# Performance work log

Hardware: AMD Instinct MI355X
Metric: run time of the kernel (lower is better)

The kernel has to match this reference:

```python
import jax, jax.numpy as jnp
from jax import lax
import numpy as np

NUM_HEADS = 16
NUM_HEADS_KV = 4
HEAD_DIM = 128
D_CONV = 4
ROT_DIM = 128
ROT_BASE = 10000.0
CAUSAL = True


def setup_inputs() -> dict:
    key = jax.random.key(0)
    ks = jax.random.split(key, 7)
    B, S, E = 2, 2048, 2048
    QKV = HEAD_DIM * (NUM_HEADS + 2 * NUM_HEADS_KV)  # 3072
    return {
        "x": jax.random.normal(ks[0], (B, S, E), jnp.float32),
        "W_in": jax.random.normal(ks[1], (QKV, E), jnp.float32) * 0.02,
        "b_in": jax.random.normal(ks[2], (QKV,), jnp.float32) * 0.02,
        "conv_w": jax.random.normal(ks[3], (QKV, D_CONV), jnp.float32) * 0.1,
        "conv_b": jax.random.normal(ks[4], (QKV,), jnp.float32) * 0.02,
        "W_out": jax.random.normal(ks[5], (E, NUM_HEADS * HEAD_DIM), jnp.float32) * 0.02,
        "b_out": jax.random.normal(ks[6], (E,), jnp.float32) * 0.02,
    }


def _rotary(x, cos, sin):
    # x: [B,S,H,D], non-interleaved rotary over first ROT_DIM dims (here full D)
    x1, x2 = x[..., : ROT_DIM // 2], x[..., ROT_DIM // 2 : ROT_DIM]
    c = cos[None, :, None, :]
    s = sin[None, :, None, :]
    rot = jnp.concatenate([x1 * c - x2 * s, x2 * c + x1 * s], axis=-1)
    return jnp.concatenate([rot, x[..., ROT_DIM:]], axis=-1)


def reference(x, W_in, b_in, conv_w, conv_b, W_out, b_out):
    B, S, E = x.shape
    QKV = conv_w.shape[0]
    # fused in-projection
    qkv = jnp.einsum("bse,fe->bsf", x, W_in) + b_in  # [B,S,QKV]
    # depthwise causal conv1d (left pad d_conv-1, equivalent to torch pad+trim)
    qkv_t = jnp.transpose(qkv, (0, 2, 1))  # [B,C,S]
    qkv_t = jnp.pad(qkv_t, ((0, 0), (0, 0), (D_CONV - 1, 0)))
    conv = lax.conv_general_dilated(
        qkv_t, conv_w[:, None, :], window_strides=(1,), padding="VALID",
        feature_group_count=QKV, dimension_numbers=("NCH", "OIH", "NCH"))
    qkv = jnp.transpose(conv + conv_b[None, :, None], (0, 2, 1))  # [B,S,QKV]
    # split q / kv
    q_dim = NUM_HEADS * HEAD_DIM
    q = qkv[..., :q_dim].reshape(B, S, NUM_HEADS, HEAD_DIM)
    kv = qkv[..., q_dim:].reshape(B, S, 2, NUM_HEADS_KV, HEAD_DIM)
    k, v = kv[:, :, 0], kv[:, :, 1]
    # rotary embedding on q and k
    t = jnp.arange(S, dtype=jnp.float32)
    inv_freq = 1.0 / (ROT_BASE ** (jnp.arange(0, ROT_DIM, 2, dtype=jnp.float32) / ROT_DIM))
    freqs = t[:, None] * inv_freq[None, :]  # [S, ROT_DIM/2]
    cos, sin = jnp.cos(freqs), jnp.sin(freqs)
    q = _rotary(q, cos, sin)
    k = _rotary(k, cos, sin)
    # GQA: repeat kv heads
    rep = NUM_HEADS // NUM_HEADS_KV
    k = jnp.repeat(k, rep, axis=2)  # [B,S,H,D]
    v = jnp.repeat(v, rep, axis=2)
    scale = 1.0 / jnp.sqrt(jnp.float32(HEAD_DIM))
    scores = jnp.einsum("bshd,bthd->bhst", q, k) * scale  # [B,H,S,S]
    if CAUSAL:
        mask = jnp.tril(jnp.ones((S, S), dtype=bool))
        scores = jnp.where(mask[None, None], scores, jnp.finfo(scores.dtype).min)
    attn = jax.nn.softmax(scores, axis=-1)
    ctx = jnp.einsum("bhst,bthd->bshd", attn, v).reshape(B, S, q_dim)
    return jnp.einsum("bsf,ef->bse", ctx, W_out) + b_out
```

## Files before the change

### kernel.cpp

```cpp
#include <hip/hip_runtime.h>
#include <hip/hip_bf16.h>

#define B_   2
#define S_   2048
#define E_   2048
#define QKV_ 3072
#define NH   16
#define NKV  4
#define HD   128
#define SL   16

typedef __attribute__((ext_vector_type(8))) short bf16x8;
typedef __attribute__((ext_vector_type(4))) float f32x4;
typedef unsigned short u16;
typedef unsigned int   u32;

__device__ __forceinline__ float bf2f(u16 u) {
  union { u32 i; float f; } v; v.i = ((u32)u) << 16; return v.f;
}
__device__ __forceinline__ u16 f2bf(float f) {
  union { float f; u32 u; } v; v.f = f;
  return (u16)((v.u + 0x7FFFu + ((v.u >> 16) & 1u)) >> 16);
}
__device__ __forceinline__ u32 pkbf(float a, float b) {
  __hip_bfloat162 h = __float22bfloat162_rn(float2{a, b});
  u32 r; __builtin_memcpy(&r, &h, 4); return r;
}
__device__ __forceinline__ float ex2(float x) { return __builtin_amdgcn_exp2f(x); }
__device__ __forceinline__ u32 shf(u32 v, int l) { return (u32)__shfl((int)v, l); }
__device__ __forceinline__ void load_lds16(const u16* g, u16* l) {
  __builtin_amdgcn_global_load_lds((const __attribute__((address_space(1))) void*)g,
                                   (__attribute__((address_space(3))) void*)l, 16, 0, 0);
}

__global__ __launch_bounds__(256) void f2b3(const float* __restrict__ x,
                                            const float* __restrict__ wi,
                                            const float* __restrict__ wo,
                                            u16* __restrict__ xb,
                                            u16* __restrict__ wib,
                                            u16* __restrict__ wob) {
  const int i = blockIdx.x * 256 + threadIdx.x;
  const float* src; u16* dst; int j;
  if (i < 2097152)            { src = x;  dst = xb;  j = i; }
  else if (i < 2097152 + 1572864) { src = wi; dst = wib; j = i - 2097152; }
  else                        { src = wo; dst = wob; j = i - 3670016; }
  const float4 v = ((const float4*)src)[j];
  ushort4 o;
  o.x = f2bf(v.x); o.y = f2bf(v.y); o.z = f2bf(v.z); o.w = f2bf(v.w);
  ((ushort4*)dst)[j] = o;
}

template <int OUT_BF16>
__global__ __launch_bounds__(512, 2) void gemm256(const u16* __restrict__ A,
                                                  const u16* __restrict__ Bm,
                                                  const float* __restrict__ bias,
                                                  void* __restrict__ C,
                                                  int M, int N, int K) {
  __shared__ u16 sm[2][2][256 * 64];
  const int tid = threadIdx.x;
  const int lane = tid & 63;
  const int wave = tid >> 6;
  const int wm = wave >> 2, wn = wave & 3;
  const int L15 = lane & 15, Lq = lane >> 4;
  const int m0 = blockIdx.y * 256, n0 = blockIdx.x * 256;
  const int NT = K >> 6;

  const int srow = tid >> 3;
  const int sdst = (tid & 7) * 8;
  const int ssrc = ((tid & 7) ^ (srow & 7)) * 8;

  f32x4 acc[8][4] = {};
  bf16x8 af[4][2], bf0[2][2], bf1[2][2];

#define STAGE_A(BUF, TC, H, J)                                                    \
  { const int row_ = (H) * 128 + (J) * 64 + srow;                                 \
    load_lds16(A + (size_t)(m0 + row_) * K + (TC) * 64 + ssrc,                    \
               &sm[BUF][0][row_ * 64 + sdst]); }
#define STAGE_B(BUF, TC, H, J)                                                    \
  { const int row_ = (H) * 128 + (J) * 64 + srow;                                 \
    load_lds16(Bm + (size_t)(n0 + row_) * K + (TC) * 64 + ssrc,                   \
               &sm[BUF][1][row_ * 64 + sdst]); }
#define RD_A(BUF, MS, MF, KK)                                                     \
  (*(const bf16x8*)&sm[BUF][0][(wm * 128 + (MS) * 64 + (MF) * 16 + L15) * 64 +    \
        ((((KK) * 4 + Lq) ^ ((wm * 128 + (MS) * 64 + (MF) * 16 + L15) & 7)) * 8)])
#define RD_B(BUF, NS, NF, KK)                                                     \
  (*(const bf16x8*)&sm[BUF][1][(wn * 64 + (NS) * 32 + (NF) * 16 + L15) * 64 +     \
        ((((KK) * 4 + Lq) ^ ((wn * 64 + (NS) * 32 + (NF) * 16 + L15) & 7)) * 8)])

#define MFMA_QUAD(MS, NS, BF)                                                     \
  __builtin_amdgcn_s_setprio(1);                                                  \
  _Pragma("unroll")                                                               \
  for (int kk = 0; kk < 2; ++kk)                                                  \
    _Pragma("unroll")                                                             \
    for (int mf = 0; mf < 4; ++mf)                                                \
      _Pragma("unroll")                                                           \
      for (int nf = 0; nf < 2; ++nf)                                              \
        acc[MS * 4 + mf][NS * 2 + nf] = __builtin_amdgcn_mfma_f32_16x16x32_bf16(  \
            af[mf][kk], BF[nf][kk], acc[MS * 4 + mf][NS * 2 + nf], 0, 0, 0);      \
  __builtin_amdgcn_s_setprio(0);

#define TILE_BODY(BUF, TT)                                                        \
  {                                                                               \
    _Pragma("unroll")                                                             \
    for (int mf = 0; mf < 4; ++mf)                                                \
      _Pragma("unroll")                                                           \
      for (int kk = 0; kk < 2; ++kk) af[mf][kk] = RD_A(BUF, 0, mf, kk);           \
    _Pragma("unroll")                                                             \
    for (int nf = 0; nf < 2; ++nf)                                                \
      _Pragma("unroll")                                                           \
      for (int kk = 0; kk < 2; ++kk) bf0[nf][kk] = RD_B(BUF, 0, nf, kk);          \
    if ((TT) + 1 < NT) { STAGE_A(BUF ^ 1, (TT) + 1, 1, 0)                         \
                         STAGE_A(BUF ^ 1, (TT) + 1, 1, 1) }                       \
    __builtin_amdgcn_s_barrier();                                                 \
    MFMA_QUAD(0, 0, bf0)                                                          \
    __builtin_amdgcn_s_barrier();                                                 \
    _Pragma("unroll")                                                             \
    for (int nf = 0; nf < 2; ++nf)                                                \
      _Pragma("unroll")                                                           \
      for (int kk = 0; kk < 2; ++kk) bf1[nf][kk] = RD_B(BUF, 1, nf, kk);          \
    if ((TT) + 1 < NT) { STAGE_B(BUF ^ 1, (TT) + 1, 1, 0)                         \
                         STAGE_B(BUF ^ 1, (TT) + 1, 1, 1) }                       \
    __builtin_amdgcn_s_barrier();                                                 \
    MFMA_QUAD(0, 1, bf1)                                                          \
    __builtin_amdgcn_s_barrier();                                                 \
    _Pragma("unroll")                                                             \
    for (int mf = 0; mf < 4; ++mf)                                                \
      _Pragma("unroll")                                                           \
      for (int kk = 0; kk < 2; ++kk) af[mf][kk] = RD_A(BUF, 1, mf, kk);           \
    if ((TT) + 2 < NT) { STAGE_B(BUF, (TT) + 2, 0, 0)                             \
                         STAGE_B(BUF, (TT) + 2, 0, 1) }                           \
    __builtin_amdgcn_s_barrier();                                                 \
    MFMA_QUAD(1, 0, bf0)                                                          \
    __builtin_amdgcn_s_barrier();                                                 \
    if ((TT) + 2 < NT) {                                                          \
      STAGE_A(BUF, (TT) + 2, 0, 0)                                                \
      STAGE_A(BUF, (TT) + 2, 0, 1)                                                \
      asm volatile("s_waitcnt vmcnt(4)" ::: "memory");                            \
    } else {                                                                      \
      asm volatile("s_waitcnt vmcnt(0)" ::: "memory");                            \
    }                                                                             \
    __builtin_amdgcn_s_barrier();                                                 \
    MFMA_QUAD(1, 1, bf1)                                                          \
    __builtin_amdgcn_s_barrier();                                                 \
  }

  STAGE_A(0, 0, 0, 0) STAGE_A(0, 0, 0, 1)
  STAGE_B(0, 0, 0, 0) STAGE_B(0, 0, 0, 1)
  STAGE_A(0, 0, 1, 0) STAGE_A(0, 0, 1, 1)
  STAGE_B(0, 0, 1, 0) STAGE_B(0, 0, 1, 1)
  STAGE_B(1, 1, 0, 0) STAGE_B(1, 1, 0, 1)
  STAGE_A(1, 1, 0, 0) STAGE_A(1, 1, 0, 1)
  asm volatile("s_waitcnt vmcnt(4)" ::: "memory");
  __builtin_amdgcn_s_barrier();

  for (int T = 0; T < NT; T += 2) {
    TILE_BODY(0, T)
    TILE_BODY(1, T + 1)
  }
#undef TILE_BODY
#undef MFMA_QUAD
#undef RD_B
#undef RD_A
#undef STAGE_B
#undef STAGE_A

#pragma unroll
  for (int ms = 0; ms < 2; ++ms)
#pragma unroll
    for (int mf = 0; mf < 4; ++mf) {
      const int grow0 = m0 + wm * 128 + ms * 64 + mf * 16 + Lq * 4;
#pragma unroll
      for (int ns = 0; ns < 2; ++ns)
#pragma unroll
        for (int nf = 0; nf < 2; ++nf) {
          const int gcol = n0 + wn * 64 + ns * 32 + nf * 16 + L15;
          const float bv = bias[gcol];
          const f32x4 v = acc[ms * 4 + mf][ns * 2 + nf];
#pragma unroll
          for (int r = 0; r < 4; ++r) {
            const float o = v[r] + bv;
            if (OUT_BF16) ((u16*)C)[(size_t)(grow0 + r) * N + gcol] = f2bf(o);
            else          ((float*)C)[(size_t)(grow0 + r) * N + gcol] = o;
          }
        }
    }
}

__global__ __launch_bounds__(512, 2) void gemm_n128(const u16* __restrict__ A,
                                                    const u16* __restrict__ Bm,
                                                    const float* __restrict__ bias,
                                                    float* __restrict__ C,
                                                    int M, int N, int K) {
  __shared__ u16 sm[2][24576];
  const int tid = threadIdx.x, lane = tid & 63, wave = tid >> 6;
  const int wm = wave >> 1, wn = wave & 1;
  const int L15 = lane & 15, Lq = lane >> 4;
  const int m0 = blockIdx.y * 256, n0 = blockIdx.x * 128;
  const int NT = K >> 6;

  const int srow = tid >> 3;
  const int sdst = (tid & 7) * 8;
  const int ssrc = ((tid & 7) ^ (srow & 7)) * 8;

  f32x4 acc[4][4] = {};

#define STAGE6(BUF, TC)                                                           \
  {                                                                               \
    _Pragma("unroll")                                                             \
    for (int c = 0; c < 4; ++c) {                                                 \
      const int row_ = c * 64 + srow;                                             \
      load_lds16(A + (size_t)(m0 + row_) * K + (TC) * 64 + ssrc,                  \
                 &sm[BUF][row_ * 64 + sdst]);                                     \
    }                                                                             \
    _Pragma("unroll")                                                             \
    for (int c = 0; c < 2; ++c) {                                                 \
      const int row_ = c * 64 + srow;                                             \
      load_lds16(Bm + (size_t)(n0 + row_) * K + (TC) * 64 + ssrc,                 \
                 &sm[BUF][16384 + row_ * 64 + sdst]);                             \
    }                                                                             \
  }

#define COMPUTE(BUF)                                                              \
  {                                                                               \
    bf16x8 af[4][2], bfr[4][2];                                                   \
    _Pragma("unroll")                                                             \
    for (int mf = 0; mf < 4; ++mf)                                                \
      _Pragma("unroll")                                                           \
      for (int kk = 0; kk < 2; ++kk) {                                            \
        const int row_ = wm * 64 + mf * 16 + L15;                                 \
        const int u_ = (kk * 4 + Lq) ^ (row_ & 7);                                \
        af[mf][kk] = *(const bf16x8*)&sm[BUF][row_ * 64 + u_ * 8];                \
      }                                                                           \
    _Pragma("unroll")                                                             \
    for (int nf = 0; nf < 4; ++nf)                                                \
      _Pragma("unroll")                                                           \
      for (int kk = 0; kk < 2; ++kk) {                                            \
        const int row_ = wn * 64 + nf * 16 + L15;                                 \
        const int u_ = (kk * 4 + Lq) ^ (row_ & 7);                                \
        bfr[nf][kk] = *(const bf16x8*)&sm[BUF][16384 + row_ * 64 + u_ * 8];       \
      }                                                                           \
    __builtin_amdgcn_s_setprio(1);                                                \
    _Pragma("unroll")                                                             \
    for (int kk = 0; kk < 2; ++kk)                                                \
      _Pragma("unroll")                                                           \
      for (int mf = 0; mf < 4; ++mf)                                              \
        _Pragma("unroll")                                                         \
        for (int nf = 0; nf < 4; ++nf)                                            \
          acc[mf][nf] = __builtin_amdgcn_mfma_f32_16x16x32_bf16(                  \
              af[mf][kk], bfr[nf][kk], acc[mf][nf], 0, 0, 0);                     \
    __builtin_amdgcn_s_setprio(0);                                                \
    __builtin_amdgcn_s_barrier();                                                 \
  }

  STAGE6(0, 0)
  for (int T = 0; T < NT; T += 2) {
    if (T + 1 < NT) {
      STAGE6(1, T + 1)
      asm volatile("s_waitcnt vmcnt(6)" ::: "memory");
    } else {
      asm volatile("s_waitcnt vmcnt(0)" ::: "memory");
    }
    __builtin_amdgcn_s_barrier();
    COMPUTE(0)
    if (T + 2 < NT) {
      STAGE6(0, T + 2)
      asm volatile("s_waitcnt vmcnt(6)" ::: "memory");
    } else {
      asm volatile("s_waitcnt vmcnt(0)" ::: "memory");
    }
    __builtin_amdgcn_s_barrier();
    COMPUTE(1)
  }
#undef COMPUTE
#undef STAGE6

#pragma unroll
  for (int mf = 0; mf < 4; ++mf) {
    const int grow0 = m0 + wm * 64 + mf * 16 + Lq * 4;
#pragma unroll
    for (int nf = 0; nf < 4; ++nf) {
      const int gcol = n0 + wn * 64 + nf * 16 + L15;
      const float bv = bias[gcol];
#pragma unroll
      for (int r = 0; r < 4; ++r)
        C[(size_t)(grow0 + r) * N + gcol] = acc[mf][nf][r] + bv;
    }
  }
}

__global__ __launch_bounds__(256) void conv_rope(const u16* __restrict__ qkv,
                                                 const float* __restrict__ cw,
                                                 const float* __restrict__ cb,
                                                 u16* __restrict__ qo,
                                                 u16* __restrict__ ko,
                                                 u16* __restrict__ vtmp) {
  const int blk = blockIdx.x;
  const int b = blk >> 7;
  const int s0 = (blk & 127) * SL;
  const u16* qb = qkv + (size_t)b * S_ * QKV_;

  for (int u = threadIdx.x; u < 896; u += 256) {
    if (u < 640) {
      const int hs = u >> 5, ip = u & 31, i = ip * 2;
      int f1; u16* outbase; float scale;
      if (hs < 16) {
        f1 = hs * HD + i;
        outbase = qo + (size_t)(b * NH + hs) * S_ * HD;
        scale = 0.08838834764831845f * 1.4426950408889634f;
      } else {
        f1 = NH * HD + (hs - 16) * HD + i;
        outbase = ko + (size_t)(b * NKV + (hs - 16)) * S_ * HD;
        scale = 1.0f;
      }
      const float invf0 = powf(10000.0f, -(float)i * (1.0f / 64.0f));
      const float invf1 = powf(10000.0f, -(float)(i + 1) * (1.0f / 64.0f));
      const int f2 = f1 + 64;
      const float4 wA0 = *(const float4*)&cw[f1 * 4];
      const float4 wA1 = *(const float4*)&cw[(f1 + 1) * 4];
      const float4 wB0 = *(const float4*)&cw[f2 * 4];
      const float4 wB1 = *(const float4*)&cw[(f2 + 1) * 4];
      const float cA0 = cb[f1], cA1 = cb[f1 + 1], cB0 = cb[f2], cB1 = cb[f2 + 1];
      float A0[3], A1[3], B0[3], B1[3];
#pragma unroll
      for (int j = 0; j < 3; ++j) {
        const int t = s0 - 3 + j;
        if (t >= 0) {
          const u32 pa = *(const u32*)&qb[(size_t)t * QKV_ + f1];
          const u32 pb = *(const u32*)&qb[(size_t)t * QKV_ + f2];
          A0[j] = bf2f((u16)pa); A1[j] = bf2f((u16)(pa >> 16));
          B0[j] = bf2f((u16)pb); B1[j] = bf2f((u16)(pb >> 16));
        } else { A0[j] = A1[j] = B0[j] = B1[j] = 0.f; }
      }
      for (int s = s0; s < s0 + SL; ++s) {
        const u32 pa = *(const u32*)&qb[(size_t)s * QKV_ + f1];
        const u32 pb = *(const u32*)&qb[(size_t)s * QKV_ + f2];
        const float nA0 = bf2f((u16)pa), nA1 = bf2f((u16)(pa >> 16));
        const float nB0 = bf2f((u16)pb), nB1 = bf2f((u16)(pb >> 16));
        const float x1a = cA0 + wA0.x * A0[0] + wA0.y * A0[1] + wA0.z * A0[2] + wA0.w * nA0;
        const float x1b = cA1 + wA1.x * A1[0] + wA1.y * A1[1] + wA1.z * A1[2] + wA1.w * nA1;
        const float x2a = cB0 + wB0.x * B0[0] + wB0.y * B0[1] + wB0.z * B0[2] + wB0.w * nB0;
        const float x2b = cB1 + wB1.x * B1[0] + wB1.y * B1[1] + wB1.z * B1[2] + wB1.w * nB1;
        float sn0, cs0, sn1, cs1;
        sincosf((float)s * invf0, &sn0, &cs0);
        sincosf((float)s * invf1, &sn1, &cs1);
        u16* outp = outbase + (size_t)s * HD;
        *(u32*)&outp[i]      = pkbf((x1a * cs0 - x2a * sn0) * scale,
                                    (x1b * cs1 - x2b * sn1) * scale);
        *(u32*)&outp[i + 64] = pkbf((x2a * cs0 + x1a * sn0) * scale,
                                    (x2b * cs1 + x1b * sn1) * scale);
        A0[0] = A0[1]; A0[1] = A0[2]; A0[2] = nA0;
        A1[0] = A1[1]; A1[1] = A1[2]; A1[2] = nA1;
        B0[0] = B0[1]; B0[1] = B0[2]; B0[2] = nB0;
        B1[0] = B1[1]; B1[1] = B1[2]; B1[2] = nB1;
      }
    } else {
      const int vu = u - 640, h = vu >> 6, d = (vu & 63) * 2;
      const int f = (NH + NKV) * HD + h * HD + d;
      const float4 w0 = *(const float4*)&cw[f * 4];
      const float4 w1 = *(const float4*)&cw[(f + 1) * 4];
      const float c0 = cb[f], c1 = cb[f + 1];
      float V0[3], V1[3];
#pragma unroll
      for (int j = 0; j < 3; ++j) {
        const int t = s0 - 3 + j;
        if (t >= 0) {
          const u32 p = *(const u32*)&qb[(size_t)t * QKV_ + f];
          V0[j] = bf2f((u16)p); V1[j] = bf2f((u16)(p >> 16));
        } else { V0[j] = V1[j] = 0.f; }
      }
      u16* vrow = vtmp + (size_t)(b * NKV + h) * S_ * HD + d;
      for (int s = s0; s < s0 + SL; ++s) {
        const u32 p = *(const u32*)&qb[(size_t)s * QKV_ + f];
        const float n0 = bf2f((u16)p), n1 = bf2f((u16)(p >> 16));
        const float v0 = c0 + w0.x * V0[0] + w0.y * V0[1] + w0.z * V0[2] + w0.w * n0;
        const float v1 = c1 + w1.x * V1[0] + w1.y * V1[1] + w1.z * V1[2] + w1.w * n1;
        *(u32*)&vrow[(size_t)s * HD] = pkbf(v0, v1);
        V0[0] = V0[1]; V0[1] = V0[2]; V0[2] = n0;
        V1[0] = V1[1]; V1[1] = V1[2]; V1[2] = n1;
      }
    }
  }
}

__global__ __launch_bounds__(256) void vtrans(const u16* __restrict__ vin,
                                              u16* __restrict__ vout) {
  __shared__ u16 t[64][72];
  const int bh = blockIdx.z;
  const int d0 = blockIdx.y * 64;
  const int s0 = blockIdx.x * 64;
  const u16* ip = vin + ((size_t)bh * S_ + s0) * HD + d0;
  const int r = threadIdx.x >> 4, c4 = (threadIdx.x & 15) * 4;
#pragma unroll
  for (int j = 0; j < 4; ++j) {
    const ushort4 v = *(const ushort4*)&ip[(size_t)(r + j * 16) * HD + c4];
    t[c4 + 0][r + j * 16] = v.x;
    t[c4 + 1][r + j * 16] = v.y;
    t[c4 + 2][r + j * 16] = v.z;
    t[c4 + 3][r + j * 16] = v.w;
  }
  __syncthreads();
  const int dl = threadIdx.x >> 2, sc = (threadIdx.x & 3) * 16;
  u16* op = vout + (size_t)bh * HD * S_ + (size_t)(d0 + dl) * S_ + s0 + sc;
  *(bf16x8*)op       = *(const bf16x8*)&t[dl][sc];
  *(bf16x8*)(op + 8) = *(const bf16x8*)&t[dl][sc + 8];
}

__global__ __launch_bounds__(256, 2) void attn(const u16* __restrict__ q,
                                               const u16* __restrict__ k,
                                               const u16* __restrict__ v,
                                               u16* __restrict__ ctx) {
  __shared__ u16 Ks[2][64 * 128];
  __shared__ u16 Vs[128 * 64];
  const int tid = threadIdx.x, wave = tid >> 6, lane = tid & 63;
  const int L15 = lane & 15, Lq = lane >> 4;
  const int bh = blockIdx.y;
  const int b = bh >> 4, h = bh & 15, hk = h >> 2;

  const u16* kb = k + (size_t)(b * NKV + hk) * S_ * HD;
  const u16* vb = v + (size_t)(b * NKV + hk) * HD * S_;

  const int rx = L15 & 7;
  int koff[4], voff[2];
#pragma unroll
  for (int c = 0; c < 4; ++c) koff[c] = ((c * 4 + Lq) ^ rx) * 8;
#pragma unroll
  for (int kc = 0; kc < 2; ++kc) voff[kc] = ((kc * 4 + Lq) ^ rx) * 8;

  const int ksl = tid >> 4, kcp = tid & 15;
  const int vsl = tid >> 3, vcp = tid & 7;

  const int ls0 = ((Lq & 1) << 5) + L15;
  const int ls1 = ls0 + 16;
  const bool hi = (Lq & 2) != 0;

  for (int pass = 0; pass < 2; ++pass) {
    const int qt = pass ? (31 - blockIdx.x) : blockIdx.x;
    const int q0 = qt * 64;
    const int base = q0 + wave * 16;

    bf16x8 qf[4];
    {
      const u16* qp = q + ((size_t)bh * S_ + base + L15) * HD + Lq * 8;
#pragma unroll
      for (int c = 0; c < 4; ++c) qf[c] = *(const bf16x8*)(qp + c * 32);
    }

    f32x4 acc[8] = {};
    float m_i = -1e30f, l_i = 0.f;

    const int ktmax = qt + 1;

#pragma unroll
    for (int j = 0; j < 4; ++j) {
      const int krow = j * 16 + ksl;
      load_lds16(kb + (size_t)krow * HD + (kcp ^ (krow & 7)) * 8,
                 &Ks[0][(krow * 16 + kcp) * 8]);
      const int vrow = j * 32 + vsl;
      load_lds16(vb + (size_t)vrow * S_ + (vcp ^ (vrow & 7)) * 8,
                 &Vs[(vrow * 8 + vcp) * 8]);
    }
    __syncthreads();

    for (int kt = 0; kt < ktmax; ++kt) {
      const int k0 = kt * 64;
      const int cur = kt & 1;
      if (kt > 0) {
#pragma unroll
        for (int j = 0; j < 4; ++j) {
          const int vrow = j * 32 + vsl;
          load_lds16(vb + (size_t)vrow * S_ + k0 + (vcp ^ (vrow & 7)) * 8,
                     &Vs[(vrow * 8 + vcp) * 8]);
        }
      }
      if (kt + 1 < ktmax) {
        const int kn = k0 + 64;
#pragma unroll
        for (int j = 0; j < 4; ++j) {
          const int krow = j * 16 + ksl;
          load_lds16(kb + (size_t)(kn + krow) * HD + (kcp ^ (krow & 7)) * 8,
                     &Ks[cur ^ 1][(krow * 16 + kcp) * 8]);
        }
      }
      f32x4 sc[4];
#pragma unroll
      for (int nt = 0; nt < 4; ++nt) sc[nt] = f32x4{0.f, 0.f, 0.f, 0.f};
#pragma unroll
      for (int nt = 0; nt < 4; ++nt) {
#pragma unroll
        for (int c = 0; c < 4; ++c) {
          const bf16x8 kf = *(const bf16x8*)&Ks[cur][(nt * 16 + L15) * 128 + koff[c]];
          sc[nt] = __builtin_amdgcn_mfma_f32_16x16x32_bf16(kf, qf[c], sc[nt], 0, 0, 0);
        }
      }
      if (k0 + 63 > base) {
#pragma unroll
        for (int nt = 0; nt < 4; ++nt)
#pragma unroll
          for (int r = 0; r < 4; ++r) {
            const int kidx = k0 + nt * 16 + Lq * 4 + r;
            if (kidx > base + L15) sc[nt][r] = -1e30f;
          }
      }
      float mloc = fmaxf(fmaxf(fmaxf(sc[0][0], sc[0][1]), fmaxf(sc[0][2], sc[0][3])),
                         fmaxf(fmaxf(sc[1][0], sc[1][1]), fmaxf(sc[1][2], sc[1][3])));
      mloc = fmaxf(mloc,
                   fmaxf(fmaxf(fmaxf(sc[2][0], sc[2][1]), fmaxf(sc[2][2], sc[2][3])),
                         fmaxf(fmaxf(sc[3][0], sc[3][1]), fmaxf(sc[3][2], sc[3][3]))));
      mloc = fmaxf(mloc, __shfl_xor(mloc, 16));
      mloc = fmaxf(mloc, __shfl_xor(mloc, 32));
      const bool defer = __all(mloc - m_i <= 8.f);
      if (!defer) {
        const float mnew = fmaxf(m_i, mloc);
        const float alpha = ex2(m_i - mnew);
        m_i = mnew;
        l_i *= alpha;
        float aacc[4];
#pragma unroll
        for (int r = 0; r < 4; ++r) aacc[r] = __shfl(alpha, Lq * 4 + r);
#pragma unroll
        for (int dt = 0; dt < 8; ++dt)
#pragma unroll
          for (int r = 0; r < 4; ++r) acc[dt][r] *= aacc[r];
      }
      float lsum = 0.f;
#pragma unroll
      for (int nt = 0; nt < 4; ++nt)
#pragma unroll
        for (int r = 0; r < 4; ++r) {
          sc[nt][r] = ex2(sc[nt][r] - m_i);
          lsum += sc[nt][r];
        }
      lsum += __shfl_xor(lsum, 16);
      lsum += __shfl_xor(lsum, 32);
      l_i += lsum;
      u32 wA[2], wB[2], wC[2], wD[2];
      wA[0] = pkbf(sc[0][0], sc[0][1]); wA[1] = pkbf(sc[0][2], sc[0][3]);
      wB[0] = pkbf(sc[1][0], sc[1][1]); wB[1] = pkbf(sc[1][2], sc[1][3]);
      wC[0] = pkbf(sc[2][0], sc[2][1]); wC[1] = pkbf(sc[2][2], sc[2][3]);
      wD[0] = pkbf(sc[3][0], sc[3][1]); wD[1] = pkbf(sc[3][2], sc[3][3]);
      bf16x8 pa[2];
      {
        union { u32 u[4]; bf16x8 v; } t0, t1;
        u32 x0, x1;
        x0 = shf(wA[0], ls0); x1 = shf(wB[0], ls0); t0.u[0] = hi ? x1 : x0;
        x0 = shf(wA[1], ls0); x1 = shf(wB[1], ls0); t0.u[1] = hi ? x1 : x0;
        x0 = shf(wA[0], ls1); x1 = shf(wB[0], ls1); t0.u[2] = hi ? x1 : x0;
        x0 = shf(wA[1], ls1); x1 = shf(wB[1], ls1); t0.u[3] = hi ? x1 : x0;
        x0 = shf(wC[0], ls0); x1 = shf(wD[0], ls0); t1.u[0] = hi ? x1 : x0;
        x0 = shf(wC[1], ls0); x1 = shf(wD[1], ls0); t1.u[1] = hi ? x1 : x0;
        x0 = shf(wC[0], ls1); x1 = shf(wD[0], ls1); t1.u[2] = hi ? x1 : x0;
        x0 = shf(wC[1], ls1); x1 = shf(wD[1], ls1); t1.u[3] = hi ? x1 : x0;
        pa[0] = t0.v; pa[1] = t1.v;
      }
      if (kt + 1 < ktmax) asm volatile("s_waitcnt vmcnt(4)" ::: "memory");
      else                asm volatile("s_waitcnt vmcnt(0)" ::: "memory");
      __builtin_amdgcn_s_barrier();
      asm volatile("" ::: "memory");
#pragma unroll
      for (int dt = 0; dt < 8; ++dt)
#pragma unroll
        for (int kc = 0; kc < 2; ++kc) {
          const bf16x8 vf = *(const bf16x8*)&Vs[(dt * 16 + L15) * 64 + voff[kc]];
          acc[dt] = __builtin_amdgcn_mfma_f32_16x16x32_bf16(pa[kc], vf, acc[dt], 0, 0, 0);
        }
      __syncthreads();
    }
    {
      float inv[4];
#pragma unroll
      for (int r = 0; r < 4; ++r) inv[r] = 1.f / __shfl(l_i, Lq * 4 + r);
      u16* cp = ctx + ((size_t)b * S_ + base) * (NH * HD) + h * HD;
#pragma unroll
      for (int dt = 0; dt < 8; ++dt)
#pragma unroll
        for (int rp = 0; rp < 2; ++rp) {
          const u32 pk = pkbf(acc[dt][rp * 2] * inv[rp * 2],
                              acc[dt][rp * 2 + 1] * inv[rp * 2 + 1]);
          cp[(size_t)(Lq * 4 + rp * 2) * (NH * HD) + dt * 16 + L15] = (u16)pk;
          cp[(size_t)(Lq * 4 + rp * 2 + 1) * (NH * HD) + dt * 16 + L15] = (u16)(pk >> 16);
        }
    }
  }
}

extern "C" void kernel_launch(void* const* d_in, const int* in_sizes, int n_in,
                              void* d_out, int out_size, void* d_ws, size_t ws_size,
                              hipStream_t stream) {
  const float* x     = (const float*)d_in[0];
  const float* W_in  = (const float*)d_in[1];
  const float* b_in  = (const float*)d_in[2];
  const float* cw    = (const float*)d_in[3];
  const float* cb    = (const float*)d_in[4];
  const float* W_out = (const float*)d_in[5];
  const float* b_out = (const float*)d_in[6];

  char* ws = (char*)d_ws;
  u16* xb   = (u16*)(ws);
  u16* wib  = (u16*)(ws + 16777216);
  u16* wob  = (u16*)(ws + 29360128);
  u16* qkv  = (u16*)(ws + 37748736);
  u16* q_ws = (u16*)(ws + 62914560);
  u16* k_ws = (u16*)(ws + 79691776);
  u16* vt_ws= (u16*)(ws + 83886080);
  u16* vtmp = wib;
  u16* ctx  = xb;

  f2b3<<<dim3(18432), 256, 0, stream>>>(x, W_in, W_out, xb, wib, wob);
  gemm256<1><<<dim3(QKV_ / 256, (B_ * S_) / 256), 512, 0, stream>>>(
      xb, wib, b_in, (void*)qkv, B_ * S_, QKV_, E_);
  conv_rope<<<dim3(B_ * (S_ / SL)), 256, 0, stream>>>(qkv, cw, cb, q_ws, k_ws, vtmp);
  vtrans<<<dim3(S_ / 64, HD / 64, B_ * NKV), 256, 0, stream>>>(vtmp, vt_ws);
  attn<<<dim3(16, B_ * NH), 256, 0, stream>>>(q_ws, k_ws, vt_ws, ctx);
  gemm_n128<<<dim3(E_ / 128, (B_ * S_) / 256), 512, 0, stream>>>(
      ctx, wob, b_out, (float*)d_out, B_ * S_, E_, NH * HD);
}
```

Before: 320.7 us.

## Fuse V transpose into conv_rope and precompute rotary tables in shared memory

The conv_rope kernel now writes V directly in transposed [d][s] layout by accumulating 16 sequence positions per thread in registers and emitting 16-byte stores. This removes the separate vtrans kernel launch and its round trip of V through global memory. It also computes the rotary cos/sin values once per block into shared-memory tables instead of calling sincosf and powf per element. This adds a __syncthreads and shared-memory traffic, and the V path keeps more values live in registers.

```diff
diff --git a/kernel.cpp b/kernel.cpp
--- a/kernel.cpp
+++ b/kernel.cpp
@@ -293,11 +293,21 @@
                                                  const float* __restrict__ cb,
                                                  u16* __restrict__ qo,
                                                  u16* __restrict__ ko,
-                                                 u16* __restrict__ vtmp) {
+                                                 u16* __restrict__ vt) {
+  __shared__ float ctab[SL][64], stab[SL][64];
   const int blk = blockIdx.x;
   const int b = blk >> 7;
   const int s0 = (blk & 127) * SL;
   const u16* qb = qkv + (size_t)b * S_ * QKV_;
+
+  for (int idx = threadIdx.x; idx < SL * 64; idx += 256) {
+    const int sl = idx >> 6, i = idx & 63;
+    const float invf = powf(10000.0f, -(float)i * (1.0f / 64.0f));
+    float sn, cs;
+    sincosf((float)(s0 + sl) * invf, &sn, &cs);
+    ctab[sl][i] = cs; stab[sl][i] = sn;
+  }
+  __syncthreads();
 
   for (int u = threadIdx.x; u < 896; u += 256) {
     if (u < 640) {
@@ -312,8 +322,6 @@
         outbase = ko + (size_t)(b * NKV + (hs - 16)) * S_ * HD;
         scale = 1.0f;
       }
-      const float invf0 = powf(10000.0f, -(float)i * (1.0f / 64.0f));
-      const float invf1 = powf(10000.0f, -(float)(i + 1) * (1.0f / 64.0f));
       const int f2 = f1 + 64;
       const float4 wA0 = *(const float4*)&cw[f1 * 4];
       const float4 wA1 = *(const float4*)&cw[(f1 + 1) * 4];
@@ -331,7 +339,9 @@
           B0[j] = bf2f((u16)pb); B1[j] = bf2f((u16)(pb >> 16));
         } else { A0[j] = A1[j] = B0[j] = B1[j] = 0.f; }
       }
-      for (int s = s0; s < s0 + SL; ++s) {
+#pragma unroll
+      for (int sl = 0; sl < SL; ++sl) {
+        const int s = s0 + sl;
         const u32 pa = *(const u32*)&qb[(size_t)s * QKV_ + f1];
         const u32 pb = *(const u32*)&qb[(size_t)s * QKV_ + f2];
         const float nA0 = bf2f((u16)pa), nA1 = bf2f((u16)(pa >> 16));
@@ -340,14 +350,13 @@
         const float x1b = cA1 + wA1.x * A1[0] + wA1.y * A1[1] + wA1.z * A1[2] + wA1.w * nA1;
         const float x2a = cB0 + wB0.x * B0[0] + wB0.y * B0[1] + wB0.z * B0[2] + wB0.w * nB0;
         const float x2b = cB1 + wB1.x * B1[0] + wB1.y * B1[1] + wB1.z * B1[2] + wB1.w * nB1;
-        float sn0, cs0, sn1, cs1;
-        sincosf((float)s * invf0, &sn0, &cs0);
-        sincosf((float)s * invf1, &sn1, &cs1);
+        const float2 cs = *(const float2*)&ctab[sl][i];
+        const float2 sn = *(const float2*)&stab[sl][i];
         u16* outp = outbase + (size_t)s * HD;
-        *(u32*)&outp[i]      = pkbf((x1a * cs0 - x2a * sn0) * scale,
-                                    (x1b * cs1 - x2b * sn1) * scale);
-        *(u32*)&outp[i + 64] = pkbf((x2a * cs0 + x1a * sn0) * scale,
-                                    (x2b * cs1 + x1b * sn1) * scale);
+        *(u32*)&outp[i]      = pkbf((x1a * cs.x - x2a * sn.x) * scale,
+                                    (x1b * cs.y - x2b * sn.y) * scale);
+        *(u32*)&outp[i + 64] = pkbf((x2a * cs.x + x1a * sn.x) * scale,
+                                    (x2b * cs.y + x1b * sn.y) * scale);
         A0[0] = A0[1]; A0[1] = A0[2]; A0[2] = nA0;
         A1[0] = A1[1]; A1[1] = A1[2]; A1[2] = nA1;
         B0[0] = B0[1]; B0[1] = B0[2]; B0[2] = nB0;
@@ -368,41 +377,28 @@
           V0[j] = bf2f((u16)p); V1[j] = bf2f((u16)(p >> 16));
         } else { V0[j] = V1[j] = 0.f; }
       }
-      u16* vrow = vtmp + (size_t)(b * NKV + h) * S_ * HD + d;
-      for (int s = s0; s < s0 + SL; ++s) {
+      union { u32 w[8]; bf16x8 v[2]; } R0, R1;
+      float e0 = 0.f, e1 = 0.f;
+#pragma unroll
+      for (int sl = 0; sl < SL; ++sl) {
+        const int s = s0 + sl;
         const u32 p = *(const u32*)&qb[(size_t)s * QKV_ + f];
         const float n0 = bf2f((u16)p), n1 = bf2f((u16)(p >> 16));
         const float v0 = c0 + w0.x * V0[0] + w0.y * V0[1] + w0.z * V0[2] + w0.w * n0;
         const float v1 = c1 + w1.x * V1[0] + w1.y * V1[1] + w1.z * V1[2] + w1.w * n1;
-        *(u32*)&vrow[(size_t)s * HD] = pkbf(v0, v1);
+        if (sl & 1) { R0.w[sl >> 1] = pkbf(e0, v0); R1.w[sl >> 1] = pkbf(e1, v1); }
+        else        { e0 = v0; e1 = v1; }
         V0[0] = V0[1]; V0[1] = V0[2]; V0[2] = n0;
         V1[0] = V1[1]; V1[1] = V1[2]; V1[2] = n1;
       }
-    }
-  }
-}
-
-__global__ __launch_bounds__(256) void vtrans(const u16* __restrict__ vin,
-                                              u16* __restrict__ vout) {
-  __shared__ u16 t[64][72];
-  const int bh = blockIdx.z;
-  const int d0 = blockIdx.y * 64;
-  const int s0 = blockIdx.x * 64;
-  const u16* ip = vin + ((size_t)bh * S_ + s0) * HD + d0;
-  const int r = threadIdx.x >> 4, c4 = (threadIdx.x & 15) * 4;
-#pragma unroll
-  for (int j = 0; j < 4; ++j) {
-    const ushort4 v = *(const ushort4*)&ip[(size_t)(r + j * 16) * HD + c4];
-    t[c4 + 0][r + j * 16] = v.x;
-    t[c4 + 1][r + j * 16] = v.y;
-    t[c4 + 2][r + j * 16] = v.z;
-    t[c4 + 3][r + j * 16] = v.w;
-  }
-  __syncthreads();
-  const int dl = threadIdx.x >> 2, sc = (threadIdx.x & 3) * 16;
-  u16* op = vout + (size_t)bh * HD * S_ + (size_t)(d0 + dl) * S_ + s0 + sc;
-  *(bf16x8*)op       = *(const bf16x8*)&t[dl][sc];
-  *(bf16x8*)(op + 8) = *(const bf16x8*)&t[dl][sc + 8];
+      u16* vt0 = vt + ((size_t)(b * NKV + h) * HD + d) * S_ + s0;
+      *(bf16x8*)vt0        = R0.v[0];
+      *(bf16x8*)(vt0 + 8)  = R0.v[1];
+      u16* vt1 = vt0 + S_;
+      *(bf16x8*)vt1        = R1.v[0];
+      *(bf16x8*)(vt1 + 8)  = R1.v[1];
+    }
+  }
 }
 
 __global__ __launch_bounds__(256, 2) void attn(const u16* __restrict__ q,
@@ -602,14 +598,12 @@
   u16* q_ws = (u16*)(ws + 62914560);
   u16* k_ws = (u16*)(ws + 79691776);
   u16* vt_ws= (u16*)(ws + 83886080);
-  u16* vtmp = wib;
   u16* ctx  = xb;
 
   f2b3<<<dim3(18432), 256, 0, stream>>>(x, W_in, W_out, xb, wib, wob);
   gemm256<1><<<dim3(QKV_ / 256, (B_ * S_) / 256), 512, 0, stream>>>(
       xb, wib, b_in, (void*)qkv, B_ * S_, QKV_, E_);
-  conv_rope<<<dim3(B_ * (S_ / SL)), 256, 0, stream>>>(qkv, cw, cb, q_ws, k_ws, vtmp);
-  vtrans<<<dim3(S_ / 64, HD / 64, B_ * NKV), 256, 0, stream>>>(vtmp, vt_ws);
+  conv_rope<<<dim3(B_ * (S_ / SL)), 256, 0, stream>>>(qkv, cw, cb, q_ws, k_ws, vt_ws);
   attn<<<dim3(16, B_ * NH), 256, 0, stream>>>(q_ws, k_ws, vt_ws, ctx);
   gemm_n128<<<dim3(E_ / 128, (B_ * S_) / 256), 512, 0, stream>>>(
       ctx, wob, b_out, (float*)d_out, B_ * S_, E_, NH * HD);
```

New measurement: 297.1 us. -7.4%, faster.
